# Performance work log

Hardware: AMD Instinct MI355X
Metric: run time of the kernel (lower is better)

## Reference

```python
import jax, jax.numpy as jnp
import numpy as np

N = 10000      # nodes
E = 320000     # edges (avg degree 32)
SI, VI = 256, 32   # node scalar / vector channels
SE, VE = 64, 4     # edge scalar / vector channels
SO, VO = 256, 32   # output channels
IN_S = 2 * SI + SE         # 576 (self_message=True)
IN_V = 2 * VI + VE         # 68
H = max(IN_V, VO)          # 68, GBP hidden vector dim
EPS = 1e-8


def setup_inputs() -> dict:
    key = jax.random.key(0)
    ks = jax.random.split(key, 9)
    node_s = jax.random.normal(ks[0], (N, SI), jnp.float32)
    node_v = jax.random.normal(ks[1], (N, VI, 3), jnp.float32)
    edge_s = jax.random.normal(ks[2], (E, SE), jnp.float32)
    edge_v = jax.random.normal(ks[3], (E, VE, 3), jnp.float32)
    # GBP params (stored as [in, out] so y = x @ W)
    wh = jax.random.normal(ks[4], (IN_V, H), jnp.float32) / np.sqrt(IN_V)
    ws_w = jax.random.normal(ks[5], (IN_S + H, SO), jnp.float32) / np.sqrt(IN_S + H)
    ws_b = jnp.zeros((SO,), jnp.float32)
    wv = jax.random.normal(ks[6], (H, VO), jnp.float32) / np.sqrt(H)
    edge_index = jax.random.randint(ks[7], (2, E), 0, N, jnp.int64)
    return {"node_s": node_s, "node_v": node_v, "edge_s": edge_s,
            "edge_v": edge_v, "wh": wh, "ws_w": ws_w, "ws_b": ws_b,
            "wv": wv, "edge_index": edge_index}


def reference(node_s, node_v, edge_s, edge_v, wh, ws_w, ws_b, wv, edge_index):
    n = node_s.shape[0]
    src, dst = edge_index[0], edge_index[1]
    # gather + tuple_cat((s_j, v_j), edge_attr, (s_i, v_i))
    s_cat = jnp.concatenate([node_s[src], edge_s, node_s[dst]], axis=-1)   # [E, IN_S]
    v_cat = jnp.concatenate([node_v[src], edge_v, node_v[dst]], axis=-2)   # [E, IN_V, 3]
    # GBP message (activations=(None,None), no vector gate)
    v_pre = jnp.swapaxes(v_cat, -1, -2)                # [E, 3, IN_V]
    vh = v_pre @ wh                                    # [E, 3, H]
    vn = jnp.sqrt(jnp.maximum(jnp.sum(vh * vh, axis=-2), EPS))  # _norm_no_nan, [E, H]
    s_msg = jnp.concatenate([s_cat, vn], axis=-1) @ ws_w + ws_b  # [E, SO]
    v_msg = jnp.swapaxes(vh @ wv, -1, -2)              # [E, VO, 3]
    # scatter-mean to target nodes
    agg_s = jax.ops.segment_sum(s_msg, dst, num_segments=n)       # [N, SO]
    agg_v = jax.ops.segment_sum(v_msg, dst, num_segments=n)       # [N, VO, 3]
    cnt = jax.ops.segment_sum(jnp.ones((s_msg.shape[0],), s_msg.dtype), dst,
                              num_segments=n)
    cnt = jnp.maximum(cnt, 1.0)
    out_s = agg_s / cnt[:, None]
    out_v = agg_v / cnt[:, None, None]
    # _merge(s, V): flatten vector channels and append to scalars
    return jnp.concatenate([out_s, out_v.reshape(n, 3 * VO)], axis=-1)  # [N, SO+3*VO]
```

## Files before the change

kernel.cpp:

```cpp
#include <hip/hip_runtime.h>
#include <hip/hip_bf16.h>

#define N_NODES 10000
#define E_TOT   320000

typedef __attribute__((ext_vector_type(8))) short short8;
typedef __attribute__((ext_vector_type(4))) float f32x4;

#define HIST_OFF    0u
#define FILL_OFF    40000u
#define ZERO_BYTES  80000u
#define ROWPTR_OFF  80000u
#define PERM_OFF    120064u
#define PSRC_OFF    1400064u
#define PQ_OFF      2680064u
#define QV_OFF      11000064u
#define WHV4_OFF    12920064u
#define WBIG_OFF    12920576u
#define NSBF_OFF    13264640u
#define ANSB_OFF    18384640u
#define EAB_OFF     23504640u
#define AP_OFF      26704640u
#define AEV_OFF     34864640u
#define NODES_OFF   35344640u
#define AGGV_OFF    45584640u
#define FLAGS_OFF   49424640u

union BfS { __hip_bfloat16 h; short s; };
__device__ __forceinline__ short f2bf(float x) { BfS u; u.h = __float2bfloat16(x); return u.s; }
__device__ __forceinline__ float bf(short x) { BfS u; u.s = x; return __bfloat162float(u.h); }
__device__ __forceinline__ float ldin(const void* p, int f32m, long i) {
  return f32m ? ((const float*)p)[i] : __bfloat162float(((const __hip_bfloat16*)p)[i]);
}
__device__ __forceinline__ int get_ei(const void* p, int i64m, long i) {
  return i64m ? (int)(((const long long*)p)[i]) : ((const int*)p)[i];
}

__global__ __launch_bounds__(256) void detect_kernel(
    const unsigned short* __restrict__ ns_u16,
    const int* __restrict__ ei_i32, int* __restrict__ flags)
{
  __shared__ int cf, ci;
  if (threadIdx.x == 0) { cf = 0; ci = 0; }
  __syncthreads();
  int c1 = 0;
  for (int i = threadIdx.x; i < 8192; i += 256) {
    unsigned e = (ns_u16[2 * i] >> 7) & 0xFF;
    if (e < 100 || e > 140) c1++;
  }
  int c2 = 0;
  for (int i = threadIdx.x; i < 4096; i += 256)
    if (ei_i32[2 * i + 1] != 0) c2++;
  atomicAdd(&cf, c1); atomicAdd(&ci, c2);
  __syncthreads();
  if (threadIdx.x == 0) {
    flags[0] = (cf > 512) ? 1 : 0;
    flags[1] = (ci < 100) ? 1 : 0;
  }
}

__global__ __launch_bounds__(256) void hist_kernel(
    const void* __restrict__ edge_index, const int* __restrict__ flags,
    int* __restrict__ hist)
{
  const int i64m = flags[1];
  int e = blockIdx.x * 256 + threadIdx.x;
  int dst = get_ei(edge_index, i64m, (long)E_TOT + e);
  atomicAdd(&hist[dst], 1);
}

__global__ __launch_bounds__(256) void scan_kernel(
    const int* __restrict__ hist, int* __restrict__ rowptr)
{
  __shared__ int part[256];
  int tid = threadIdx.x;
  int base = tid * 40;
  int s = 0;
  for (int i = 0; i < 40; ++i) { int idx = base + i; if (idx < N_NODES) s += hist[idx]; }
  part[tid] = s;
  __syncthreads();
  for (int off = 1; off < 256; off <<= 1) {
    int v = (tid >= off) ? part[tid - off] : 0;
    __syncthreads();
    part[tid] += v;
    __syncthreads();
  }
  int run = (tid > 0) ? part[tid - 1] : 0;
  for (int i = 0; i < 40; ++i) {
    int idx = base + i;
    if (idx < N_NODES) { rowptr[idx] = run; run += hist[idx]; }
  }
  if (tid == 255) rowptr[N_NODES] = run;
}

__global__ __launch_bounds__(256) void permute_kernel(
    const void* __restrict__ edge_index, const int* __restrict__ flags,
    const int* __restrict__ rowptr, int* __restrict__ fill,
    int* __restrict__ perm, int* __restrict__ psrc)
{
  const int i64m = flags[1];
  int e = blockIdx.x * 256 + threadIdx.x;
  int dst = get_ei(edge_index, i64m, (long)E_TOT + e);
  int src = get_ei(edge_index, i64m, e);
  int pos = rowptr[dst] + atomicAdd(&fill[dst], 1);
  perm[pos] = e; psrc[pos] = src;
}

__global__ __launch_bounds__(256) void prep_kernel(
    const void* __restrict__ ws_w, const void* __restrict__ wh,
    const void* __restrict__ wv, const int* __restrict__ flags,
    short* __restrict__ Wbig, float* __restrict__ whv4)
{
  const int f32m = flags[0];
  int b = blockIdx.x, tid = threadIdx.x;
  if (b < 672) {
    int flat = b * 256 + tid;
    int o = flat / 672, k = flat % 672;
    short v = 0;
    if (k < 320)      v = f2bf(ldin(ws_w, f32m, (long)k * 256 + o));
    else if (k < 388) v = f2bf(ldin(ws_w, f32m, (long)(576 + k - 320) * 256 + o));
    else if (k >= 416) v = f2bf(ldin(ws_w, f32m, (long)(k - 96) * 256 + o));
    Wbig[flat] = v;
  } else if (tid < 128) {
    int q = tid / 32, c = tid % 32;
    float acc = 0.f;
    for (int h = 0; h < 68; ++h)
      acc += ldin(wh, f32m, (32 + q) * 68 + h) * ldin(wv, f32m, h * 32 + c);
    whv4[tid] = acc;
  }
}

__global__ __launch_bounds__(256) void nsconv_kernel(
    const void* __restrict__ node_s, const int* __restrict__ flags,
    short* __restrict__ ns_bf)
{
  const int f32m = flags[0];
  int i = blockIdx.x * 256 + threadIdx.x;
  ns_bf[i] = f2bf(ldin(node_s, f32m, i));
}

__global__ __launch_bounds__(256) void node_pre(
    const void* __restrict__ node_v, const void* __restrict__ wh,
    const void* __restrict__ wv, const int* __restrict__ flags,
    short* __restrict__ PQ, short* __restrict__ QV)
{
  const int f32m = flags[0];
  int n0 = blockIdx.x * 4, tid = threadIdx.x;
  __shared__ float nv[4][96];
  __shared__ float pq[4][408];
  for (int i = tid; i < 4 * 96; i += 256) nv[i / 96][i % 96] = ldin(node_v, f32m, (long)n0 * 96 + i);
  __syncthreads();
  for (int o = tid; o < 4 * 408; o += 256) {
    int i = o / 408, r0 = o % 408;
    int part = r0 / 204, r = r0 % 204, d = r / 68, h = r % 68;
    int cbase = part ? 36 : 0;
    float acc = 0.f;
#pragma unroll
    for (int c = 0; c < 32; ++c)
      acc += nv[i][c * 3 + d] * ldin(wh, f32m, (cbase + c) * 68 + h);
    pq[i][r0] = acc;
  }
  __syncthreads();
  for (int o = tid; o < 4 * 416; o += 256) {
    int i = o / 416, k = o % 416, part = k / 208, r = k % 208;
    PQ[(long)(n0 + i) * 416 + k] = (r < 204) ? f2bf(pq[i][part * 204 + r]) : (short)0;
  }
  for (int o = tid; o < 4 * 96; o += 256) {
    int i = o / 96, r = o % 96, d = r / 32, c = r % 32;
    float acc = 0.f;
    for (int h = 0; h < 68; ++h)
      acc += pq[i][204 + d * 68 + h] * ldin(wv, f32m, h * 32 + c);
    QV[(long)(n0 + i) * 96 + r] = f2bf(acc);
  }
}

__global__ __launch_bounds__(256) void edge_node(
    const void* __restrict__ edge_v, const void* __restrict__ edge_s,
    const void* __restrict__ wh, const int* __restrict__ flags,
    const int* __restrict__ rowptr, const int* __restrict__ perm,
    const int* __restrict__ psrc, const short* __restrict__ PQ,
    const short* __restrict__ nsb,
    short* __restrict__ ANSb, short* __restrict__ EAb,
    float* __restrict__ AP, float* __restrict__ AEV)
{
  const int f32m = flags[0];
  const int n = blockIdx.x, tid = threadIdx.x;
  const int beg = rowptr[n], deg = rowptr[n + 1] - beg;
  __shared__ float Qs[204];
  __shared__ float whs4[272];
  __shared__ __align__(16) short PsL[8 * 208];
  __shared__ float evL[8 * 12];
  __shared__ float esL[8 * 64];
  __shared__ float vnL[8 * 68];
  __shared__ int svL[8], eidL[8];
  for (int i = tid; i < 204; i += 256) Qs[i] = bf(PQ[(long)n * 416 + 208 + i]);
  for (int i = tid; i < 272; i += 256) whs4[i] = ldin(wh, f32m, (32 + i / 68) * 68 + i % 68);
  float ansc = 0.f, apc = 0.f, aev = 0.f, aesc = 0.f, avnc = 0.f;
  const int pe = tid >> 5, pc = tid & 31;
  for (int c0 = 0; c0 < deg; c0 += 8) {
    int m = min(8, deg - c0);
    __syncthreads();
    if (tid < m) { svL[tid] = psrc[beg + c0 + tid]; eidL[tid] = perm[beg + c0 + tid]; }
    __syncthreads();
    if (pe < m && pc < 26)
      *(short8*)&PsL[pe * 208 + pc * 8] = *(const short8*)&PQ[(long)svL[pe] * 416 + pc * 8];
    for (int i = tid; i < m * 12; i += 256)
      evL[i] = ldin(edge_v, f32m, (long)eidL[i / 12] * 12 + i % 12);
    for (int i = tid; i < m * 64; i += 256)
      esL[i] = ldin(edge_s, f32m, (long)eidL[i >> 6] * 64 + (i & 63));
    for (int e = 0; e < m; ++e)
      ansc += bf(nsb[(long)svL[e] * 256 + tid]);
    __syncthreads();
#pragma unroll
    for (int j = 0; j < 3; ++j) {
      int h = pc + 32 * j;
      if (pe < m && h < 68) {
        float ss = 0.f;
#pragma unroll
        for (int d = 0; d < 3; ++d) {
          float v = bf(PsL[pe * 208 + d * 68 + h]) + Qs[d * 68 + h]
                  + evL[pe * 12 + d]     * whs4[h]       + evL[pe * 12 + 3 + d] * whs4[68 + h]
                  + evL[pe * 12 + 6 + d] * whs4[136 + h] + evL[pe * 12 + 9 + d] * whs4[204 + h];
          ss += v * v;
        }
        vnL[pe * 68 + h] = sqrtf(fmaxf(ss, 1e-8f));
      }
    }
    if (tid < 204) { for (int e = 0; e < m; ++e) apc += bf(PsL[e * 208 + tid]); }
    else if (tid < 216) { int c = tid - 204; for (int e = 0; e < m; ++e) aev += evL[e * 12 + c]; }
    if (tid < 64)  { for (int e = 0; e < m; ++e) aesc += esL[e * 64 + tid]; }
    __syncthreads();
    if (tid < 68)  { for (int e = 0; e < m; ++e) avnc += vnL[e * 68 + tid]; }
  }
  float inv = 1.f / fmaxf((float)deg, 1.f);
  ANSb[(long)n * 256 + tid] = f2bf(ansc * inv);
  if (tid < 204) AP[(long)n * 204 + tid] = apc;
  else if (tid < 216) AEV[(long)n * 12 + tid - 204] = aev;
  if (tid < 64) EAb[(long)n * 160 + tid] = f2bf(aesc * inv);
  if (tid < 68) EAb[(long)n * 160 + 64 + tid] = f2bf(avnc * inv);
  if (tid >= 132 && tid < 160) EAb[(long)n * 160 + tid] = 0;
}

__global__ __launch_bounds__(256) void node_gemm(
    const short* __restrict__ ANSb, const short* __restrict__ EAb,
    const short* __restrict__ nsb, const short* __restrict__ Wbig,
    float* __restrict__ NodeS)
{
  __shared__ __align__(16) short Xs[64 * 40];
  __shared__ __align__(16) short Ws[256 * 40];
  const int tid = threadIdx.x;
  const int n0 = blockIdx.x * 64;
  const int lane = tid & 63, wave = tid >> 6;
  const int frow = lane & 15, fk = (lane >> 4) * 8, q = lane >> 4;
  f32x4 acc[4][4];
#pragma unroll
  for (int ri = 0; ri < 4; ++ri)
#pragma unroll
    for (int ci = 0; ci < 4; ++ci)
      acc[ri][ci] = (f32x4){0.f, 0.f, 0.f, 0.f};
  const int se = tid >> 2, sq = tid & 3;
  const int rn = min(n0 + se, N_NODES - 1);
  for (int s = 0; s < 21; ++s) {
    short8 xv;
    if (s < 8)       xv = *(const short8*)&ANSb[(long)rn * 256 + s * 32 + sq * 8];
    else if (s < 13) xv = *(const short8*)&EAb[(long)rn * 160 + (s - 8) * 32 + sq * 8];
    else             xv = *(const short8*)&nsb[(long)rn * 256 + (s - 13) * 32 + sq * 8];
    *(short8*)&Xs[se * 40 + sq * 8] = xv;
#pragma unroll
    for (int it = 0; it < 4; ++it) {
      int flat = it * 256 + tid;
      int nn = flat >> 2, qq = flat & 3;
      *(short8*)&Ws[nn * 40 + qq * 8] = *(const short8*)&Wbig[nn * 672 + s * 32 + qq * 8];
    }
    __syncthreads();
    short8 a[4];
#pragma unroll
    for (int ri = 0; ri < 4; ++ri)
      a[ri] = *(const short8*)&Xs[(ri * 16 + frow) * 40 + fk];
#pragma unroll
    for (int ci = 0; ci < 4; ++ci) {
      int nn = wave * 64 + ci * 16 + frow;
      short8 b = *(const short8*)&Ws[nn * 40 + fk];
#pragma unroll
      for (int ri = 0; ri < 4; ++ri)
        acc[ri][ci] = __builtin_amdgcn_mfma_f32_16x16x32_bf16(a[ri], b, acc[ri][ci], 0, 0, 0);
    }
    __syncthreads();
  }
#pragma unroll
  for (int ri = 0; ri < 4; ++ri)
#pragma unroll
    for (int rr = 0; rr < 4; ++rr) {
      int row = n0 + ri * 16 + q * 4 + rr;
      if (row < N_NODES) {
#pragma unroll
        for (int ci = 0; ci < 4; ++ci) {
          int col = wave * 64 + ci * 16 + (lane & 15);
          NodeS[(long)row * 256 + col] = acc[ri][ci][rr];
        }
      }
    }
}

__global__ __launch_bounds__(256) void nodev_kernel(
    const float* __restrict__ AP, const float* __restrict__ AEV,
    const void* __restrict__ wv, const float* __restrict__ whv4,
    const int* __restrict__ flags, float* __restrict__ agg_v)
{
  const int f32m = flags[0];
  int n0 = blockIdx.x * 4, tid = threadIdx.x;
  __shared__ float wvs[68 * 32];
  __shared__ float wh4s[128];
  __shared__ float APs[4][204];
  __shared__ float AEVs[4][12];
  for (int i = tid; i < 2176; i += 256) wvs[i] = ldin(wv, f32m, i);
  if (tid < 128) wh4s[tid] = whv4[tid];
  for (int i = tid; i < 816; i += 256) APs[i / 204][i % 204] = AP[(long)n0 * 204 + i];
  if (tid < 48) AEVs[tid / 12][tid % 12] = AEV[(long)n0 * 12 + tid];
  __syncthreads();
  for (int o = tid; o < 384; o += 256) {
    int i = o / 96, r = o % 96, c = r / 3, d = r % 3;
    float acc = AEVs[i][d] * wh4s[c] + AEVs[i][3 + d] * wh4s[32 + c]
              + AEVs[i][6 + d] * wh4s[64 + c] + AEVs[i][9 + d] * wh4s[96 + c];
    for (int h = 0; h < 68; ++h)
      acc += APs[i][d * 68 + h] * wvs[h * 32 + c];
    agg_v[(long)(n0 + i) * 96 + r] = acc;
  }
}

__global__ __launch_bounds__(256) void finalize(
    const float* __restrict__ NodeS, const float* __restrict__ agg_v,
    const int* __restrict__ rowptr, const short* __restrict__ QV,
    const void* __restrict__ ws_b, const int* __restrict__ flags,
    void* __restrict__ out)
{
  const int f32m = flags[0];
  int flat = blockIdx.x * 256 + threadIdx.x;
  int n = flat / 352, j = flat % 352;
  int deg = rowptr[n + 1] - rowptr[n];
  float v;
  if (j < 256) {
    v = (deg > 0) ? (NodeS[(long)n * 256 + j] + ldin(ws_b, f32m, j)) : 0.f;
  } else {
    int m = j - 256, ch = m / 3, d = m % 3;
    float inv = 1.f / fmaxf((float)deg, 1.f);
    v = agg_v[(long)n * 96 + m] * inv;
    if (deg > 0) v += bf(QV[(long)n * 96 + d * 32 + ch]);
  }
  if (f32m) ((float*)out)[flat] = v;
  else      ((__hip_bfloat16*)out)[flat] = __float2bfloat16(v);
}

extern "C" void kernel_launch(void* const* d_in, const int* in_sizes, int n_in,
                              void* d_out, int out_size, void* d_ws, size_t ws_size,
                              hipStream_t stream) {
  const void* node_s = d_in[0];
  const void* node_v = d_in[1];
  const void* edge_s = d_in[2];
  const void* edge_v = d_in[3];
  const void* wh     = d_in[4];
  const void* ws_w   = d_in[5];
  const void* ws_b   = d_in[6];
  const void* wv     = d_in[7];
  const void* edge_index = d_in[8];

  char* ws = (char*)d_ws;
  int*   hist  = (int*)(ws + HIST_OFF);
  int*   fill  = (int*)(ws + FILL_OFF);
  int*   rowptr= (int*)(ws + ROWPTR_OFF);
  int*   perm  = (int*)(ws + PERM_OFF);
  int*   psrc  = (int*)(ws + PSRC_OFF);
  short* PQ    = (short*)(ws + PQ_OFF);
  short* QV    = (short*)(ws + QV_OFF);
  float* whv4  = (float*)(ws + WHV4_OFF);
  short* Wbig  = (short*)(ws + WBIG_OFF);
  short* ns_bf = (short*)(ws + NSBF_OFF);
  short* ANSb  = (short*)(ws + ANSB_OFF);
  short* EAb   = (short*)(ws + EAB_OFF);
  float* AP    = (float*)(ws + AP_OFF);
  float* AEV   = (float*)(ws + AEV_OFF);
  float* NodeS = (float*)(ws + NODES_OFF);
  float* agg_v = (float*)(ws + AGGV_OFF);
  int*   flags = (int*)(ws + FLAGS_OFF);

  hipMemsetAsync(d_ws, 0, ZERO_BYTES, stream);
  detect_kernel<<<1, 256, 0, stream>>>((const unsigned short*)node_s,
                                       (const int*)edge_index, flags);
  hist_kernel<<<1250, 256, 0, stream>>>(edge_index, flags, hist);
  scan_kernel<<<1, 256, 0, stream>>>(hist, rowptr);
  permute_kernel<<<1250, 256, 0, stream>>>(edge_index, flags, rowptr, fill,
                                           perm, psrc);
  prep_kernel<<<673, 256, 0, stream>>>(ws_w, wh, wv, flags, Wbig, whv4);
  nsconv_kernel<<<10000, 256, 0, stream>>>(node_s, flags, ns_bf);
  node_pre<<<2500, 256, 0, stream>>>(node_v, wh, wv, flags, PQ, QV);
  edge_node<<<10000, 256, 0, stream>>>(edge_v, edge_s, wh, flags, rowptr,
                                       perm, psrc, PQ, ns_bf,
                                       ANSb, EAb, AP, AEV);
  node_gemm<<<157, 256, 0, stream>>>(ANSb, EAb, ns_bf, Wbig, NodeS);
  nodev_kernel<<<2500, 256, 0, stream>>>(AP, AEV, wv, whv4, flags, agg_v);
  finalize<<<13750, 256, 0, stream>>>(NodeS, agg_v, rowptr, QV, ws_b,
                                      flags, d_out);
}
```

Before: 506.8 us.

## Process each destination node with one wavefront instead of a block, using an interleaved PQ layout

The per-node edge aggregation kernel now assigns one 64-lane wavefront per destination node, four nodes per block, in place of a whole 256-thread block. Edges are walked one at a time with register accumulators, so the shared-memory staging and the several __syncthreads per 8-edge chunk go away. The PQ buffer is re-laid out so each hidden channel's three xyz components sit together (stride 4), which lets a lane fetch its values with one vector load. AP is written in the same h-major order and nodev is updated to read it that way. The kernel is templated on input precision, and workspace offsets are moved so NodeS reuses the early scratch region. The cost is a serial per-edge loop inside each wave with little memory-level parallelism per node.

Result: faster. 488.3 us (-3.7%).

```diff
diff --git a/kernel.cpp b/kernel.cpp
--- a/kernel.cpp
+++ b/kernel.cpp
@@ -5,6 +5,7 @@
 #define E_TOT   320000
 
 typedef __attribute__((ext_vector_type(8))) short short8;
+typedef __attribute__((ext_vector_type(4))) short s16x4;
 typedef __attribute__((ext_vector_type(4))) float f32x4;
 
 #define HIST_OFF    0u
@@ -14,17 +15,17 @@
 #define PERM_OFF    120064u
 #define PSRC_OFF    1400064u
 #define PQ_OFF      2680064u
-#define QV_OFF      11000064u
-#define WHV4_OFF    12920064u
-#define WBIG_OFF    12920576u
-#define NSBF_OFF    13264640u
-#define ANSB_OFF    18384640u
-#define EAB_OFF     23504640u
-#define AP_OFF      26704640u
-#define AEV_OFF     34864640u
-#define NODES_OFF   35344640u
-#define AGGV_OFF    45584640u
-#define FLAGS_OFF   49424640u
+#define QV_OFF      12280064u
+#define WHV4_OFF    14200064u
+#define WBIG_OFF    14200576u
+#define NSBF_OFF    14544640u
+#define ANSB_OFF    19664640u
+#define EAB_OFF     24784640u
+#define AP_OFF      27984640u
+#define AEV_OFF     36144640u
+#define AGGV_OFF    36624640u
+#define FLAGS_OFF   40464640u
+#define NODES_OFF   120064u
 
 union BfS { __hip_bfloat16 h; short s; };
 __device__ __forceinline__ short f2bf(float x) { BfS u; u.h = __float2bfloat16(x); return u.s; }
@@ -161,9 +162,16 @@
     pq[i][r0] = acc;
   }
   __syncthreads();
-  for (int o = tid; o < 4 * 416; o += 256) {
-    int i = o / 416, k = o % 416, part = k / 208, r = k % 208;
-    PQ[(long)(n0 + i) * 416 + k] = (r < 204) ? f2bf(pq[i][part * 204 + r]) : (short)0;
+  for (int o = tid; o < 4 * 480; o += 256) {
+    int i = o / 480, k = o % 480;
+    short v = 0;
+    if (k < 272) {
+      int h = k >> 2, d = k & 3;
+      if (d < 3) v = f2bf(pq[i][d * 68 + h]);
+    } else if (k < 476) {
+      v = f2bf(pq[i][204 + (k - 272)]);
+    }
+    PQ[(long)(n0 + i) * 480 + k] = v;
   }
   for (int o = tid; o < 4 * 96; o += 256) {
     int i = o / 96, r = o % 96, d = r / 32, c = r % 32;
@@ -174,7 +182,102 @@
   }
 }
 
-__global__ __launch_bounds__(256) void edge_node(
+template <int F32M>
+__device__ __forceinline__ void edge_body(
+    const void* __restrict__ edge_v, const void* __restrict__ edge_s,
+    const void* __restrict__ wh,
+    const int* __restrict__ rowptr, const int* __restrict__ perm,
+    const int* __restrict__ psrc, const short* __restrict__ PQ,
+    const short* __restrict__ nsb,
+    short* __restrict__ ANSb, short* __restrict__ EAb,
+    float* __restrict__ AP, float* __restrict__ AEV)
+{
+  const int lane = threadIdx.x & 63;
+  const int n = blockIdx.x * 4 + (threadIdx.x >> 6);
+  const int beg = rowptr[n], deg = rowptr[n + 1] - beg;
+  const bool has2 = (lane < 4);
+  const int h2 = 64 + lane;
+  const float w4a0 = ldin(wh, F32M, 32 * 68 + lane);
+  const float w4a1 = ldin(wh, F32M, 33 * 68 + lane);
+  const float w4a2 = ldin(wh, F32M, 34 * 68 + lane);
+  const float w4a3 = ldin(wh, F32M, 35 * 68 + lane);
+  const float w4b0 = has2 ? ldin(wh, F32M, 32 * 68 + h2) : 0.f;
+  const float w4b1 = has2 ? ldin(wh, F32M, 33 * 68 + h2) : 0.f;
+  const float w4b2 = has2 ? ldin(wh, F32M, 34 * 68 + h2) : 0.f;
+  const float w4b3 = has2 ? ldin(wh, F32M, 35 * 68 + h2) : 0.f;
+  const short* pqQ = PQ + (long)n * 480 + 272;
+  const float qa0 = bf(pqQ[0 * 68 + lane]);
+  const float qa1 = bf(pqQ[1 * 68 + lane]);
+  const float qa2 = bf(pqQ[2 * 68 + lane]);
+  const float qb0 = has2 ? bf(pqQ[0 * 68 + h2]) : 0.f;
+  const float qb1 = has2 ? bf(pqQ[1 * 68 + h2]) : 0.f;
+  const float qb2 = has2 ? bf(pqQ[2 * 68 + h2]) : 0.f;
+  float an0 = 0.f, an1 = 0.f, an2 = 0.f, an3 = 0.f;
+  float ap0 = 0.f, ap1 = 0.f, ap2 = 0.f;
+  float bq0 = 0.f, bq1 = 0.f, bq2 = 0.f;
+  float avna = 0.f, avnb = 0.f, aes = 0.f, aev = 0.f;
+  for (int e = 0; e < deg; ++e) {
+    const int sv  = psrc[beg + e];
+    const int eid = perm[beg + e];
+    float ev0, ev1, ev2, ev3, ev4, ev5, ev6, ev7, ev8, ev9, evA, evB;
+    if (F32M) {
+      const float* evp = (const float*)edge_v + (long)eid * 12;
+      f32x4 a = *(const f32x4*)evp;
+      f32x4 b = *(const f32x4*)(evp + 4);
+      f32x4 c = *(const f32x4*)(evp + 8);
+      ev0 = a.x; ev1 = a.y; ev2 = a.z; ev3 = a.w;
+      ev4 = b.x; ev5 = b.y; ev6 = b.z; ev7 = b.w;
+      ev8 = c.x; ev9 = c.y; evA = c.z; evB = c.w;
+    } else {
+      const short* evp = (const short*)edge_v + (long)eid * 12;
+      s16x4 a = *(const s16x4*)evp;
+      s16x4 b = *(const s16x4*)(evp + 4);
+      s16x4 c = *(const s16x4*)(evp + 8);
+      ev0 = bf(a.x); ev1 = bf(a.y); ev2 = bf(a.z); ev3 = bf(a.w);
+      ev4 = bf(b.x); ev5 = bf(b.y); ev6 = bf(b.z); ev7 = bf(b.w);
+      ev8 = bf(c.x); ev9 = bf(c.y); evA = bf(c.z); evB = bf(c.w);
+    }
+    const short* ps = PQ + (long)sv * 480;
+    s16x4 pv = *(const s16x4*)(ps + lane * 4);
+    const float pa0 = bf(pv.x), pa1 = bf(pv.y), pa2 = bf(pv.z);
+    s16x4 nvv = *(const s16x4*)(nsb + (long)sv * 256 + lane * 4);
+    an0 += bf(nvv.x); an1 += bf(nvv.y); an2 += bf(nvv.z); an3 += bf(nvv.w);
+    aes += ldin(edge_s, F32M, (long)eid * 64 + lane);
+    if (lane < 12) aev += ldin(edge_v, F32M, (long)eid * 12 + lane);
+    float v0 = pa0 + qa0 + ev0 * w4a0 + ev3 * w4a1 + ev6 * w4a2 + ev9 * w4a3;
+    float v1 = pa1 + qa1 + ev1 * w4a0 + ev4 * w4a1 + ev7 * w4a2 + evA * w4a3;
+    float v2 = pa2 + qa2 + ev2 * w4a0 + ev5 * w4a1 + ev8 * w4a2 + evB * w4a3;
+    avna += sqrtf(fmaxf(v0 * v0 + v1 * v1 + v2 * v2, 1e-8f));
+    ap0 += pa0; ap1 += pa1; ap2 += pa2;
+    if (has2) {
+      s16x4 p2 = *(const s16x4*)(ps + h2 * 4);
+      const float pb0 = bf(p2.x), pb1 = bf(p2.y), pb2 = bf(p2.z);
+      float u0 = pb0 + qb0 + ev0 * w4b0 + ev3 * w4b1 + ev6 * w4b2 + ev9 * w4b3;
+      float u1 = pb1 + qb1 + ev1 * w4b0 + ev4 * w4b1 + ev7 * w4b2 + evA * w4b3;
+      float u2 = pb2 + qb2 + ev2 * w4b0 + ev5 * w4b1 + ev8 * w4b2 + evB * w4b3;
+      avnb += sqrtf(fmaxf(u0 * u0 + u1 * u1 + u2 * u2, 1e-8f));
+      bq0 += pb0; bq1 += pb1; bq2 += pb2;
+    }
+  }
+  const float inv = 1.f / fmaxf((float)deg, 1.f);
+  s16x4 av;
+  av.x = f2bf(an0 * inv); av.y = f2bf(an1 * inv);
+  av.z = f2bf(an2 * inv); av.w = f2bf(an3 * inv);
+  *(s16x4*)(ANSb + (long)n * 256 + lane * 4) = av;
+  EAb[(long)n * 160 + lane] = f2bf(aes * inv);
+  EAb[(long)n * 160 + 64 + lane] = f2bf(avna * inv);
+  if (has2) EAb[(long)n * 160 + 128 + lane] = f2bf(avnb * inv);
+  if (lane >= 4 && lane < 32) EAb[(long)n * 160 + 128 + lane] = 0;
+  float* app = AP + (long)n * 204 + lane * 3;
+  app[0] = ap0; app[1] = ap1; app[2] = ap2;
+  if (has2) {
+    float* apb = AP + (long)n * 204 + h2 * 3;
+    apb[0] = bq0; apb[1] = bq1; apb[2] = bq2;
+  }
+  if (lane < 12) AEV[(long)n * 12 + lane] = aev;
+}
+
+__global__ __launch_bounds__(256) void edge_wave(
     const void* __restrict__ edge_v, const void* __restrict__ edge_s,
     const void* __restrict__ wh, const int* __restrict__ flags,
     const int* __restrict__ rowptr, const int* __restrict__ perm,
@@ -183,62 +286,12 @@
     short* __restrict__ ANSb, short* __restrict__ EAb,
     float* __restrict__ AP, float* __restrict__ AEV)
 {
-  const int f32m = flags[0];
-  const int n = blockIdx.x, tid = threadIdx.x;
-  const int beg = rowptr[n], deg = rowptr[n + 1] - beg;
-  __shared__ float Qs[204];
-  __shared__ float whs4[272];
-  __shared__ __align__(16) short PsL[8 * 208];
-  __shared__ float evL[8 * 12];
-  __shared__ float esL[8 * 64];
-  __shared__ float vnL[8 * 68];
-  __shared__ int svL[8], eidL[8];
-  for (int i = tid; i < 204; i += 256) Qs[i] = bf(PQ[(long)n * 416 + 208 + i]);
-  for (int i = tid; i < 272; i += 256) whs4[i] = ldin(wh, f32m, (32 + i / 68) * 68 + i % 68);
-  float ansc = 0.f, apc = 0.f, aev = 0.f, aesc = 0.f, avnc = 0.f;
-  const int pe = tid >> 5, pc = tid & 31;
-  for (int c0 = 0; c0 < deg; c0 += 8) {
-    int m = min(8, deg - c0);
-    __syncthreads();
-    if (tid < m) { svL[tid] = psrc[beg + c0 + tid]; eidL[tid] = perm[beg + c0 + tid]; }
-    __syncthreads();
-    if (pe < m && pc < 26)
-      *(short8*)&PsL[pe * 208 + pc * 8] = *(const short8*)&PQ[(long)svL[pe] * 416 + pc * 8];
-    for (int i = tid; i < m * 12; i += 256)
-      evL[i] = ldin(edge_v, f32m, (long)eidL[i / 12] * 12 + i % 12);
-    for (int i = tid; i < m * 64; i += 256)
-      esL[i] = ldin(edge_s, f32m, (long)eidL[i >> 6] * 64 + (i & 63));
-    for (int e = 0; e < m; ++e)
-      ansc += bf(nsb[(long)svL[e] * 256 + tid]);
-    __syncthreads();
-#pragma unroll
-    for (int j = 0; j < 3; ++j) {
-      int h = pc + 32 * j;
-      if (pe < m && h < 68) {
-        float ss = 0.f;
-#pragma unroll
-        for (int d = 0; d < 3; ++d) {
-          float v = bf(PsL[pe * 208 + d * 68 + h]) + Qs[d * 68 + h]
-                  + evL[pe * 12 + d]     * whs4[h]       + evL[pe * 12 + 3 + d] * whs4[68 + h]
-                  + evL[pe * 12 + 6 + d] * whs4[136 + h] + evL[pe * 12 + 9 + d] * whs4[204 + h];
-          ss += v * v;
-        }
-        vnL[pe * 68 + h] = sqrtf(fmaxf(ss, 1e-8f));
-      }
-    }
-    if (tid < 204) { for (int e = 0; e < m; ++e) apc += bf(PsL[e * 208 + tid]); }
-    else if (tid < 216) { int c = tid - 204; for (int e = 0; e < m; ++e) aev += evL[e * 12 + c]; }
-    if (tid < 64)  { for (int e = 0; e < m; ++e) aesc += esL[e * 64 + tid]; }
-    __syncthreads();
-    if (tid < 68)  { for (int e = 0; e < m; ++e) avnc += vnL[e * 68 + tid]; }
-  }
-  float inv = 1.f / fmaxf((float)deg, 1.f);
-  ANSb[(long)n * 256 + tid] = f2bf(ansc * inv);
-  if (tid < 204) AP[(long)n * 204 + tid] = apc;
-  else if (tid < 216) AEV[(long)n * 12 + tid - 204] = aev;
-  if (tid < 64) EAb[(long)n * 160 + tid] = f2bf(aesc * inv);
-  if (tid < 68) EAb[(long)n * 160 + 64 + tid] = f2bf(avnc * inv);
-  if (tid >= 132 && tid < 160) EAb[(long)n * 160 + tid] = 0;
+  if (flags[0])
+    edge_body<1>(edge_v, edge_s, wh, rowptr, perm, psrc, PQ, nsb,
+                 ANSb, EAb, AP, AEV);
+  else
+    edge_body<0>(edge_v, edge_s, wh, rowptr, perm, psrc, PQ, nsb,
+                 ANSb, EAb, AP, AEV);
 }
 
 __global__ __launch_bounds__(256) void node_gemm(
@@ -323,7 +376,7 @@
     float acc = AEVs[i][d] * wh4s[c] + AEVs[i][3 + d] * wh4s[32 + c]
               + AEVs[i][6 + d] * wh4s[64 + c] + AEVs[i][9 + d] * wh4s[96 + c];
     for (int h = 0; h < 68; ++h)
-      acc += APs[i][d * 68 + h] * wvs[h * 32 + c];
+      acc += APs[i][h * 3 + d] * wvs[h * 32 + c];
     agg_v[(long)(n0 + i) * 96 + r] = acc;
   }
 }
@@ -393,9 +446,9 @@
   prep_kernel<<<673, 256, 0, stream>>>(ws_w, wh, wv, flags, Wbig, whv4);
   nsconv_kernel<<<10000, 256, 0, stream>>>(node_s, flags, ns_bf);
   node_pre<<<2500, 256, 0, stream>>>(node_v, wh, wv, flags, PQ, QV);
-  edge_node<<<10000, 256, 0, stream>>>(edge_v, edge_s, wh, flags, rowptr,
-                                       perm, psrc, PQ, ns_bf,
-                                       ANSb, EAb, AP, AEV);
+  edge_wave<<<2500, 256, 0, stream>>>(edge_v, edge_s, wh, flags, rowptr,
+                                      perm, psrc, PQ, ns_bf,
+                                      ANSb, EAb, AP, AEV);
   node_gemm<<<157, 256, 0, stream>>>(ANSb, EAb, ns_bf, Wbig, NodeS);
   nodev_kernel<<<2500, 256, 0, stream>>>(AP, AEV, wv, whv4, flags, agg_v);
   finalize<<<13750, 256, 0, stream>>>(NodeS, agg_v, rowptr, QV, ws_b,
```
